# Kernel tuning notes

Measured on AMD Instinct MI355X. Metric: run time of the kernel, lower is better.

## Reference

```python
import jax, jax.numpy as jnp
import numpy as np

WIDTH = 36
N = WIDTH * WIDTH          # 1296 graph nodes per patch
SIGMA = 0.01               # weight_sigma
ZMAX = 0.01                # support_zmax
U_MIN, U_MAX = 0.001, 1.0
N_ITERS = 9                # 1 initial qpsolve + 8 glr refinements


def _build_graph():
    # 4-connected grid graph on WIDTH x WIDTH pixels -> incidence matrix H [E, N]
    nodes = np.arange(N).reshape(WIDTH, WIDTH)
    i0 = np.concatenate([nodes[:, :-1].ravel(), nodes[:-1, :].ravel()])
    i1 = np.concatenate([nodes[:, 1:].ravel(), nodes[1:, :].ravel()])
    E = i0.shape[0]  # 2520
    H = np.zeros((E, N), np.float32)
    H[np.arange(E), i0] = 1.0
    H[np.arange(E), i1] = -1.0
    return i0.astype(np.int32), i1.astype(np.int32), H


def setup_inputs() -> dict:
    key = jax.random.key(0)
    ks = jax.random.split(key, 6)
    B = 2
    i0, i1, H = _build_graph()
    std = 0.02  # weights_init_normal
    return {
        "xf": jax.random.normal(ks[0], (B, 3, WIDTH, WIDTH), jnp.float32),
        "u_param": jax.random.uniform(ks[1], (1,), jnp.float32),
        "H": jnp.asarray(H),
        "cw_in": std * jax.random.normal(ks[2], (32, 3, 3, 3), jnp.float32),
        "b_in": jnp.zeros((32,), jnp.float32),
        "cw_mid": std * jax.random.normal(ks[3], (5, 32, 32, 3, 3), jnp.float32),
        "b_mid": jnp.zeros((5, 32), jnp.float32),
        "cw_out": std * jax.random.normal(ks[4], (6, 32, 3, 3), jnp.float32),
        "b_out": jnp.zeros((6,), jnp.float32),
        "idx0": jnp.asarray(i0),
        "idx1": jnp.asarray(i1),
    }


def _conv(x, w, b):
    y = jax.lax.conv_general_dilated(x, w, (1, 1), "SAME",
                                     dimension_numbers=("NCHW", "OIHW", "NCHW"))
    return y + b[None, :, None, None]


def _cnnf(x, cw_in, b_in, cw_mid, b_mid, cw_out, b_out):
    h = jax.nn.relu(_conv(x, cw_in, b_in))
    for i in range(cw_mid.shape[0]):
        h = jax.nn.relu(_conv(h, cw_mid[i], b_mid[i]))
    return _conv(h, cw_out, b_out)


def _forward(xf, u_param, H, cw_in, b_in, cw_mid, b_mid, cw_out, b_out, idx0, idx1):
    B, C = xf.shape[0], xf.shape[1]
    Ne = idx0.shape[0]
    u = jnp.clip(u_param, U_MIN, U_MAX)[0]  # cnnu == uu(): scalar u, clamped

    y = xf.reshape(B, C, N, 1)
    # edge weights from deep features: w = exp(-sum_f (H f)^2 / sigma^2)
    feat = _cnnf(xf, cw_in, b_in, cw_mid, b_mid, cw_out, b_out).reshape(B, 6, N, 1)
    Fs = jnp.einsum("en,bfno->bfeo", H, feat) ** 2          # [B,6,E,1]
    w = jnp.exp(-Fs.sum(axis=1) / (SIGMA ** 2))              # [B,E,1]
    wv = jnp.broadcast_to(w[:, None, :, 0], (B, C, Ne))      # repeat over channels

    eye = jnp.eye(N, dtype=xf.dtype)
    base = jnp.zeros((B, C, N, N), xf.dtype)                 # base_W

    def step(y):
        z = jnp.einsum("en,bcno->bceo", H, y)                # per-edge diffs [B,C,E,1]
        za = jnp.abs(z[..., 0])                              # [B,C,E]
        Wm = base.at[:, :, idx0, idx1].set(wv).at[:, :, idx1, idx0].set(wv)
        Zm = base.at[:, :, idx0, idx1].set(za).at[:, :, idx1, idx0].set(za)
        Zm = jnp.maximum(Zm, ZMAX)
        Lm = Wm / Zm                                         # reweighted adjacency
        deg = Lm.sum(axis=-1)                                # L @ ones(N,1)
        L = deg[..., :, None] * eye - Lm                     # graph Laplacian
        # qpsolve: GLR closed form  (I + u L) x = y
        return jnp.linalg.solve(eye + u * L, y)

    for _ in range(N_ITERS):
        y = step(y)
    return y.reshape(B, C, WIDTH, WIDTH)


def reference(xf, u_param, H, cw_in, b_in, cw_mid, b_mid, cw_out, b_out, idx0, idx1):
    return _forward(xf, u_param, H, cw_in, b_in, cw_mid, b_mid, cw_out, b_out, idx0, idx1)
```

## Files before the change

kernel.cpp:

```cpp
#include <hip/hip_runtime.h>
#include <math.h>

#define NN 1296
#define OFF 40
#define TOT (OFF + NN + 40)
#define KMAX 240
#define PXW 21

__global__ __launch_bounds__(256) void conv_in_k(
    const float* __restrict__ in, const float* __restrict__ wgt,
    const float* __restrict__ bias, float* __restrict__ out)
{
  const int gid = blockIdx.x * 256 + threadIdx.x;
  const int wid = gid >> 6, lane = gid & 63;
  if (wid >= 2 * 32 * PXW) return;
  const int px = (wid % PXW) * 64 + lane;
  const int co = __builtin_amdgcn_readfirstlane((wid / PXW) % 32);
  const int b  = __builtin_amdgcn_readfirstlane(wid / (PXW * 32));
  if (px >= NN) return;

  const int py = px / 36, pxx = px % 36;
  int offs[9]; float msk[9];
#pragma unroll
  for (int dy = 0; dy < 3; ++dy)
#pragma unroll
    for (int dx = 0; dx < 3; ++dx) {
      const int yy = py + dy - 1, xx = pxx + dx - 1;
      const bool okp = ((unsigned)yy < 36u) && ((unsigned)xx < 36u);
      offs[dy * 3 + dx] = okp ? (yy * 36 + xx) : 0;
      msk[dy * 3 + dx]  = okp ? 1.f : 0.f;
    }

  float acc = bias[co];
  const float* __restrict__ inp = in + (size_t)b * 3 * NN;
  const float* __restrict__ wB  = wgt + (size_t)co * 3 * 9;
#pragma unroll
  for (int ci = 0; ci < 3; ++ci) {
    float v[9];
#pragma unroll
    for (int k9 = 0; k9 < 9; ++k9) v[k9] = msk[k9] * inp[ci * NN + offs[k9]];
#pragma unroll
    for (int k9 = 0; k9 < 9; ++k9) acc = fmaf(v[k9], wB[ci * 9 + k9], acc);
  }
  out[(size_t)(b * 32 + co) * NN + px] = fmaxf(acc, 0.f);
}

__global__ __launch_bounds__(256) void conv_mid2_k(
    const float* __restrict__ in, const float* __restrict__ wgt,
    const float* __restrict__ bias, float* __restrict__ out)
{
  const int blk = blockIdx.x;
  const int pxg = blk % PXW;
  const int cog = (blk / PXW) & 3;
  const int b   = blk / (PXW * 4);
  const int lane = threadIdx.x & 63;
  const int ciq  = __builtin_amdgcn_readfirstlane(threadIdx.x >> 6);
  const int px   = pxg * 64 + lane;
  const bool ok  = px < NN;

  __shared__ float part[4][8][64];

  float acc[8] = {0.f, 0.f, 0.f, 0.f, 0.f, 0.f, 0.f, 0.f};
  if (ok) {
    const int py = px / 36, pxx = px % 36;
    int offs[9]; float msk[9];
#pragma unroll
    for (int dy = 0; dy < 3; ++dy)
#pragma unroll
      for (int dx = 0; dx < 3; ++dx) {
        const int yy = py + dy - 1, xx = pxx + dx - 1;
        const bool okp = ((unsigned)yy < 36u) && ((unsigned)xx < 36u);
        offs[dy * 3 + dx] = okp ? (yy * 36 + xx) : 0;
        msk[dy * 3 + dx]  = okp ? 1.f : 0.f;
      }
    const float* __restrict__ inp = in + ((size_t)b * 32 + ciq * 8) * NN;
    const float* __restrict__ wB = wgt + ((size_t)(cog * 8) * 32 + ciq * 8) * 9;
#pragma unroll
    for (int ci = 0; ci < 8; ++ci) {
      float v[9];
#pragma unroll
      for (int k9 = 0; k9 < 9; ++k9) v[k9] = msk[k9] * inp[ci * NN + offs[k9]];
#pragma unroll
      for (int t = 0; t < 8; ++t)
#pragma unroll
        for (int k9 = 0; k9 < 9; ++k9)
          acc[t] = fmaf(v[k9], wB[(t * 32 + ci) * 9 + k9], acc[t]);
    }
  }
#pragma unroll
  for (int t = 0; t < 8; ++t) part[ciq][t][lane] = acc[t];
  __syncthreads();
  if (ok) {
#pragma unroll
    for (int tt = 0; tt < 2; ++tt) {
      const int t = ciq + tt * 4;
      float s = part[0][t][lane] + part[1][t][lane]
              + part[2][t][lane] + part[3][t][lane] + bias[cog * 8 + t];
      s = fmaxf(s, 0.f);
      out[((size_t)b * 32 + cog * 8 + t) * NN + px] = s;
    }
  }
}

template<int COUT, bool RELU>
__global__ __launch_bounds__(256) void conv_mid_k(
    const float* __restrict__ in, const float* __restrict__ wgt,
    const float* __restrict__ bias, float* __restrict__ out)
{
  const int blk = blockIdx.x;
  const int pxg = blk % PXW;
  const int co  = (blk / PXW) % COUT;
  const int b   = blk / (PXW * COUT);
  const int lane = threadIdx.x & 63;
  const int ciq  = threadIdx.x >> 6;
  const int px   = pxg * 64 + lane;
  const bool ok  = px < NN;

  __shared__ float part[4][64];

  float acc = 0.f;
  if (ok) {
    const int py = px / 36, pxx = px % 36;
    int offs[9]; float msk[9];
#pragma unroll
    for (int dy = 0; dy < 3; ++dy)
#pragma unroll
      for (int dx = 0; dx < 3; ++dx) {
        const int yy = py + dy - 1, xx = pxx + dx - 1;
        const bool okp = ((unsigned)yy < 36u) && ((unsigned)xx < 36u);
        offs[dy * 3 + dx] = okp ? (yy * 36 + xx) : 0;
        msk[dy * 3 + dx]  = okp ? 1.f : 0.f;
      }
    const float* __restrict__ inp = in + ((size_t)b * 32 + ciq * 8) * NN;
    const float* __restrict__ wB  = wgt + ((size_t)co * 32 + ciq * 8) * 9;
#pragma unroll
    for (int ci = 0; ci < 8; ++ci) {
      float v[9];
#pragma unroll
      for (int k9 = 0; k9 < 9; ++k9) v[k9] = msk[k9] * inp[ci * NN + offs[k9]];
#pragma unroll
      for (int k9 = 0; k9 < 9; ++k9) acc = fmaf(v[k9], wB[ci * 9 + k9], acc);
    }
  }
  part[ciq][lane] = acc;
  __syncthreads();
  if (threadIdx.x < 64 && ok) {
    float s = part[0][lane] + part[1][lane] + part[2][lane] + part[3][lane]
            + bias[co];
    if (RELU) s = fmaxf(s, 0.f);
    out[((size_t)b * COUT + co) * NN + px] = s;
  }
}

__global__ __launch_bounds__(384) void gtv_k(
    const float* __restrict__ xf, const float* __restrict__ up,
    const float* __restrict__ feat, float* __restrict__ out)
{
  const int sys = blockIdx.x, b = sys / 3, ch = sys % 3;
  const int tid = threadIdx.x;
  const int wave = tid >> 6, lane = tid & 63;
  const bool act = tid < 324;
  const int qq = act ? tid : 0;
  const int i0 = OFF + 4 * qq;

  __shared__ __align__(16) float ysL[TOT], ahL[TOT], avL[TOT],
                                 dA[TOT], dB[TOT], dgL[TOT];
  __shared__ float red[16];

  float u = up[0]; u = fminf(fmaxf(u, 0.001f), 1.0f);

  if (tid < OFF) {
    const int t2 = OFF + NN + tid;
    ysL[tid] = 0.f; ahL[tid] = 0.f; avL[tid] = 0.f;
    dA[tid] = 0.f; dB[tid] = 0.f; dgL[tid] = 0.f;
    ysL[t2] = 0.f; ahL[t2] = 0.f; avL[t2] = 0.f;
    dA[t2] = 0.f; dB[t2] = 0.f; dgL[t2] = 0.f;
  }

  const float* __restrict__ xfB = xf + (size_t)(b * 3 + ch) * NN;
  float wh4[4] = {0.f, 0.f, 0.f, 0.f}, wv4[4] = {0.f, 0.f, 0.f, 0.f};
  if (act) {
    *(float4*)&ysL[i0] = *(const float4*)&xfB[4 * qq];
#pragma unroll
    for (int j = 0; j < 4; ++j) {
      const int n = 4 * qq + j;
      const int col = n % 36, row = n / 36;
      float sh = 0.f, sv = 0.f;
#pragma unroll
      for (int f = 0; f < 6; ++f) {
        const float* __restrict__ fp = feat + (size_t)(b * 6 + f) * NN;
        const float a = fp[n];
        if (col < 35) { const float d = a - fp[n + 1];  sh += d * d; }
        if (row < 35) { const float d = a - fp[n + 36]; sv += d * d; }
      }
      wh4[j] = (col < 35) ? expf(-sh * 1e4f) : 0.f;
      wv4[j] = (row < 35) ? expf(-sv * 1e4f) : 0.f;
    }
  }
  __syncthreads();

  float x[4] = {0.f, 0.f, 0.f, 0.f};

  for (int it = 0; it < 9; ++it) {
    float4 yv = make_float4(0,0,0,0);
    float ah[4] = {0,0,0,0}, av[4] = {0,0,0,0};
    if (act) {
      yv = *(const float4*)&ysL[i0];
      const float yR = ysL[i0 + 4];
      const float4 yD = *(const float4*)&ysL[i0 + 36];
      ah[0] = u * wh4[0] / fmaxf(fabsf(yv.x - yv.y), 0.01f);
      ah[1] = u * wh4[1] / fmaxf(fabsf(yv.y - yv.z), 0.01f);
      ah[2] = u * wh4[2] / fmaxf(fabsf(yv.z - yv.w), 0.01f);
      ah[3] = u * wh4[3] / fmaxf(fabsf(yv.w - yR  ), 0.01f);
      av[0] = u * wv4[0] / fmaxf(fabsf(yv.x - yD.x), 0.01f);
      av[1] = u * wv4[1] / fmaxf(fabsf(yv.y - yD.y), 0.01f);
      av[2] = u * wv4[2] / fmaxf(fabsf(yv.z - yD.z), 0.01f);
      av[3] = u * wv4[3] / fmaxf(fabsf(yv.w - yD.w), 0.01f);
      *(float4*)&ahL[i0] = make_float4(ah[0], ah[1], ah[2], ah[3]);
      *(float4*)&avL[i0] = make_float4(av[0], av[1], av[2], av[3]);
    }
    __syncthreads();

    float cL[4], cR[4], cU[4], cD[4], cc[4], bn[4], os[4];
    float mo = 0.f;
    if (act) {
      const float cl0 = ahL[i0 - 1];
      const float4 aU = *(const float4*)&avL[i0 - 36];
      cL[0] = cl0;  cL[1] = ah[0]; cL[2] = ah[1]; cL[3] = ah[2];
      cR[0] = ah[0]; cR[1] = ah[1]; cR[2] = ah[2]; cR[3] = ah[3];
      cU[0] = aU.x; cU[1] = aU.y; cU[2] = aU.z; cU[3] = aU.w;
      cD[0] = av[0]; cD[1] = av[1]; cD[2] = av[2]; cD[3] = av[3];
      bn[0] = yv.x; bn[1] = yv.y; bn[2] = yv.z; bn[3] = yv.w;
#pragma unroll
      for (int j = 0; j < 4; ++j) {
        os[j] = cL[j] + cR[j] + cU[j] + cD[j];
        cc[j] = 1.f + os[j];
        mo = fmaxf(mo, os[j]);
      }
      *(float4*)&dA[i0]  = yv;
      *(float4*)&dgL[i0] = make_float4(os[0], os[1], os[2], os[3]);
    } else {
#pragma unroll
      for (int j = 0; j < 4; ++j) {
        cL[j]=cR[j]=cU[j]=cD[j]=0.f; cc[j]=1.f; bn[j]=0.f; os[j]=0.f;
      }
    }
#pragma unroll
    for (int o = 32; o >= 1; o >>= 1) mo = fmaxf(mo, __shfl_xor(mo, o));
    if (lane == 0) red[wave] = mo;
    __syncthreads();

    float me = 0.f;
    if (act) {
      const float dnx3 = dgL[i0 + 4];
      const float4 dwn = *(const float4*)&dgL[i0 + 36];
      const float dn_[4] = { os[1], os[2], os[3], dnx3 };
      const float dd_[4] = { dwn.x, dwn.y, dwn.z, dwn.w };
#pragma unroll
      for (int j = 0; j < 4; ++j)
        me = fmaxf(me, os[j] + fmaxf(dn_[j], dd_[j]));
    }
#pragma unroll
    for (int o = 32; o >= 1; o >>= 1) me = fmaxf(me, __shfl_xor(me, o));
    if (lane == 0) red[8 + wave] = me;
    __syncthreads();
    if (tid == 0) {
      float m1 = red[0], m2 = red[8];
      for (int w = 1; w < 6; ++w) {
        m1 = fmaxf(m1, red[w]); m2 = fmaxf(m2, red[8 + w]);
      }
      red[14] = fminf(2.f * m1, m2);
    }
    __syncthreads();

    const float lmaxL = red[14];
    const float h     = 0.5f * lmaxL;
    const float theta = 1.f + h;
    const float del   = fmaxf(h, 1e-30f);
    const float sig1  = theta / del;
    const float rho0  = del / theta;
    const float kappa = 1.f + lmaxL;
    const float srk   = sqrtf(kappa);
    const float rc    = (srk - 1.f) / (srk + 1.f);

    float r[4], d[4];
    float rmx = 0.f;
    if (act) {
      const float dl = dA[i0 - 1], dr = dA[i0 + 4];
      const float4 u4 = *(const float4*)&dA[i0 - 36];
      const float4 d4 = *(const float4*)&dA[i0 + 36];
      const float uu[4] = {u4.x, u4.y, u4.z, u4.w};
      const float dd[4] = {d4.x, d4.y, d4.z, d4.w};
#pragma unroll
      for (int j = 0; j < 4; ++j) {
        const float nl = (j == 0) ? dl : bn[j - 1];
        const float nr = (j == 3) ? dr : bn[j + 1];
        const float Ab = cc[j] * bn[j] - cL[j] * nl - cR[j] * nr
                       - cU[j] * uu[j] - cD[j] * dd[j];
        x[j] = bn[j];
        r[j] = bn[j] - Ab;
        d[j] = r[j] / theta;
        rmx = fmaxf(rmx, fabsf(r[j]));
      }
      *(float4*)&dB[i0] = make_float4(d[0], d[1], d[2], d[3]);
    } else {
#pragma unroll
      for (int j = 0; j < 4; ++j) { r[j] = 0.f; d[j] = 0.f; x[j] = 0.f; }
    }
#pragma unroll
    for (int o = 32; o >= 1; o >>= 1) rmx = fmaxf(rmx, __shfl_xor(rmx, o));
    if (lane == 0) red[wave] = rmx;
    __syncthreads();
    if (tid == 0) {
      float m = red[0];
      for (int w = 1; w < 6; ++w) m = fmaxf(m, red[w]);
      red[9] = m;
    }
    __syncthreads();

    const float rmax = red[9];
    int kneed;
    if (rmax <= 5e-4f) kneed = 0;
    else if (rc < 1e-10f) kneed = 1;
    else {
      kneed = (int)ceilf(8.0f / (-logf(rc)));
      kneed = (kneed < 1) ? 1 : (kneed > KMAX ? KMAX : kneed);
    }

    float rho = rho0;
    float* dc = dB; float* dnx = dA;
    for (int k = 0; k < kneed; ++k) {
      const float rn = 1.f / (2.f * sig1 - rho);
      const float cd = rn * rho, cr = 2.f * rn / del;
      rho = rn;
      if (act) {
        const float dl = dc[i0 - 1], dr = dc[i0 + 4];
        const float4 u4 = *(const float4*)&dc[i0 - 36];
        const float4 d4 = *(const float4*)&dc[i0 + 36];
        const float uu[4] = {u4.x, u4.y, u4.z, u4.w};
        const float dd[4] = {d4.x, d4.y, d4.z, d4.w};
        float dn[4];
#pragma unroll
        for (int j = 0; j < 4; ++j) {
          const float nl = (j == 0) ? dl : d[j - 1];
          const float nr = (j == 3) ? dr : d[j + 1];
          const float Ad = cc[j] * d[j] - cL[j] * nl - cR[j] * nr
                         - cU[j] * uu[j] - cD[j] * dd[j];
          x[j] += d[j];
          r[j] -= Ad;
          dn[j] = cd * d[j] + cr * r[j];
        }
        *(float4*)&dnx[i0] = make_float4(dn[0], dn[1], dn[2], dn[3]);
#pragma unroll
        for (int j = 0; j < 4; ++j) d[j] = dn[j];
      }
      __syncthreads();
      float* t = dc; dc = dnx; dnx = t;
    }

    if (act) *(float4*)&ysL[i0] = make_float4(x[0], x[1], x[2], x[3]);
    __syncthreads();
  }

  if (act) *(float4*)&out[(size_t)(b * 3 + ch) * NN + 4 * qq]
      = make_float4(x[0], x[1], x[2], x[3]);
}

extern "C" void kernel_launch(void* const* d_in, const int* in_sizes, int n_in,
                              void* d_out, int out_size, void* d_ws, size_t ws_size,
                              hipStream_t stream) {
  const float* xf     = (const float*)d_in[0];
  const float* up     = (const float*)d_in[1];
  const float* cw_in  = (const float*)d_in[3];
  const float* b_in   = (const float*)d_in[4];
  const float* cw_mid = (const float*)d_in[5];
  const float* b_mid  = (const float*)d_in[6];
  const float* cw_out = (const float*)d_in[7];
  const float* b_out  = (const float*)d_in[8];

  float* ws   = (float*)d_ws;
  float* hb0  = ws;
  float* hb1  = hb0 + 82944;
  float* feat = hb1 + 82944;

  conv_in_k<<<dim3(336), dim3(256), 0, stream>>>(xf, cw_in, b_in, hb0);
  const float* src = hb0; float* dst = hb1;
  for (int i = 0; i < 5; ++i) {
    conv_mid2_k<<<dim3(2 * 4 * PXW), dim3(256), 0, stream>>>(
        src, cw_mid + i * 9216, b_mid + i * 32, dst);
    const float* t = dst; dst = (float*)src; src = t;
  }
  conv_mid_k<6, false><<<dim3(2 * 6 * PXW), dim3(256), 0, stream>>>(
      src, cw_out, b_out, feat);

  gtv_k<<<dim3(6), dim3(384), 0, stream>>>(xf, up, feat, (float*)d_out);
}
```

Before: 117.4 us.

## Add residual-based early exit to Chebyshev loop and merge reduction barriers

Stops the Chebyshev iteration early once the max residual, reduced across the block every four steps, falls below a relative tolerance, instead of always running the precomputed iteration cap. Also drops the degree scratch array by recomputing neighbour degrees from edge weights, and replaces single-thread reductions with redundant per-thread reads to remove several barriers. Costs an extra wave reduction every four iterations and makes iteration count data dependent, with looser accuracy control.

```diff
diff --git a/kernel.cpp b/kernel.cpp
--- a/kernel.cpp
+++ b/kernel.cpp
@@ -163,18 +163,15 @@
   const int qq = act ? tid : 0;
   const int i0 = OFF + 4 * qq;
 
-  __shared__ __align__(16) float ysL[TOT], ahL[TOT], avL[TOT],
-                                 dA[TOT], dB[TOT], dgL[TOT];
+  __shared__ __align__(16) float ysL[TOT], ahL[TOT], avL[TOT], dA[TOT], dB[TOT];
   __shared__ float red[16];
 
   float u = up[0]; u = fminf(fmaxf(u, 0.001f), 1.0f);
 
   if (tid < OFF) {
     const int t2 = OFF + NN + tid;
-    ysL[tid] = 0.f; ahL[tid] = 0.f; avL[tid] = 0.f;
-    dA[tid] = 0.f; dB[tid] = 0.f; dgL[tid] = 0.f;
-    ysL[t2] = 0.f; ahL[t2] = 0.f; avL[t2] = 0.f;
-    dA[t2] = 0.f; dB[t2] = 0.f; dgL[t2] = 0.f;
+    ysL[tid] = 0.f; ahL[tid] = 0.f; avL[tid] = 0.f; dA[tid] = 0.f; dB[tid] = 0.f;
+    ysL[t2] = 0.f; ahL[t2] = 0.f; avL[t2] = 0.f; dA[t2] = 0.f; dB[t2] = 0.f;
   }
 
   const float* __restrict__ xfB = xf + (size_t)(b * 3 + ch) * NN;
@@ -202,12 +199,13 @@
   float x[4] = {0.f, 0.f, 0.f, 0.f};
 
   for (int it = 0; it < 9; ++it) {
-    float4 yv = make_float4(0,0,0,0);
+    float4 yv = make_float4(0,0,0,0), yD = make_float4(0,0,0,0);
+    float yR = 0.f;
     float ah[4] = {0,0,0,0}, av[4] = {0,0,0,0};
     if (act) {
       yv = *(const float4*)&ysL[i0];
-      const float yR = ysL[i0 + 4];
-      const float4 yD = *(const float4*)&ysL[i0 + 36];
+      yR = ysL[i0 + 4];
+      yD = *(const float4*)&ysL[i0 + 36];
       ah[0] = u * wh4[0] / fmaxf(fabsf(yv.x - yv.y), 0.01f);
       ah[1] = u * wh4[1] / fmaxf(fabsf(yv.y - yv.z), 0.01f);
       ah[2] = u * wh4[2] / fmaxf(fabsf(yv.z - yv.w), 0.01f);
@@ -222,7 +220,7 @@
     __syncthreads();
 
     float cL[4], cR[4], cU[4], cD[4], cc[4], bn[4], os[4];
-    float mo = 0.f;
+    float mo = 0.f, me = 0.f;
     if (act) {
       const float cl0 = ahL[i0 - 1];
       const float4 aU = *(const float4*)&avL[i0 - 36];
@@ -237,8 +235,22 @@
         cc[j] = 1.f + os[j];
         mo = fmaxf(mo, os[j]);
       }
-      *(float4*)&dA[i0]  = yv;
-      *(float4*)&dgL[i0] = make_float4(os[0], os[1], os[2], os[3]);
+      const float ahR  = ahL[i0 + 4];
+      const float avRu = avL[i0 - 32];
+      const float avR  = avL[i0 + 4];
+      const float osR  = ah[3] + ahR + avRu + avR;
+      const float ahDl = ahL[i0 + 35];
+      const float4 ahD = *(const float4*)&ahL[i0 + 36];
+      const float4 avD = *(const float4*)&avL[i0 + 36];
+      float osD[4];
+      osD[0] = ahDl  + ahD.x + av[0] + avD.x;
+      osD[1] = ahD.x + ahD.y + av[1] + avD.y;
+      osD[2] = ahD.y + ahD.z + av[2] + avD.z;
+      osD[3] = ahD.z + ahD.w + av[3] + avD.w;
+      const float osN[4] = { os[1], os[2], os[3], osR };
+#pragma unroll
+      for (int j = 0; j < 4; ++j)
+        me = fmaxf(me, os[j] + fmaxf(osN[j], osD[j]));
     } else {
 #pragma unroll
       for (int j = 0; j < 4; ++j) {
@@ -246,34 +258,18 @@
       }
     }
 #pragma unroll
-    for (int o = 32; o >= 1; o >>= 1) mo = fmaxf(mo, __shfl_xor(mo, o));
-    if (lane == 0) red[wave] = mo;
+    for (int o = 32; o >= 1; o >>= 1) {
+      mo = fmaxf(mo, __shfl_xor(mo, o));
+      me = fmaxf(me, __shfl_xor(me, o));
+    }
+    if (lane == 0) { red[wave] = mo; red[8 + wave] = me; }
     __syncthreads();
-
-    float me = 0.f;
-    if (act) {
-      const float dnx3 = dgL[i0 + 4];
-      const float4 dwn = *(const float4*)&dgL[i0 + 36];
-      const float dn_[4] = { os[1], os[2], os[3], dnx3 };
-      const float dd_[4] = { dwn.x, dwn.y, dwn.z, dwn.w };
-#pragma unroll
-      for (int j = 0; j < 4; ++j)
-        me = fmaxf(me, os[j] + fmaxf(dn_[j], dd_[j]));
-    }
-#pragma unroll
-    for (int o = 32; o >= 1; o >>= 1) me = fmaxf(me, __shfl_xor(me, o));
-    if (lane == 0) red[8 + wave] = me;
-    __syncthreads();
-    if (tid == 0) {
-      float m1 = red[0], m2 = red[8];
-      for (int w = 1; w < 6; ++w) {
-        m1 = fmaxf(m1, red[w]); m2 = fmaxf(m2, red[8 + w]);
-      }
-      red[14] = fminf(2.f * m1, m2);
-    }
-    __syncthreads();
-
-    const float lmaxL = red[14];
+    float m1 = fmaxf(fmaxf(red[0], red[1]),
+               fmaxf(fmaxf(red[2], red[3]), fmaxf(red[4], red[5])));
+    float m2 = fmaxf(fmaxf(red[8], red[9]),
+               fmaxf(fmaxf(red[10], red[11]), fmaxf(red[12], red[13])));
+    const float lmaxL = fminf(2.f * m1, m2);
+
     const float h     = 0.5f * lmaxL;
     const float theta = 1.f + h;
     const float del   = fmaxf(h, 1e-30f);
@@ -286,15 +282,14 @@
     float r[4], d[4];
     float rmx = 0.f;
     if (act) {
-      const float dl = dA[i0 - 1], dr = dA[i0 + 4];
-      const float4 u4 = *(const float4*)&dA[i0 - 36];
-      const float4 d4 = *(const float4*)&dA[i0 + 36];
-      const float uu[4] = {u4.x, u4.y, u4.z, u4.w};
-      const float dd[4] = {d4.x, d4.y, d4.z, d4.w};
+      const float bl = ysL[i0 - 1];
+      const float4 bu = *(const float4*)&ysL[i0 - 36];
+      const float uu[4] = {bu.x, bu.y, bu.z, bu.w};
+      const float dd[4] = {yD.x, yD.y, yD.z, yD.w};
 #pragma unroll
       for (int j = 0; j < 4; ++j) {
-        const float nl = (j == 0) ? dl : bn[j - 1];
-        const float nr = (j == 3) ? dr : bn[j + 1];
+        const float nl = (j == 0) ? bl : bn[j - 1];
+        const float nr = (j == 3) ? yR : bn[j + 1];
         const float Ab = cc[j] * bn[j] - cL[j] * nl - cR[j] * nr
                        - cU[j] * uu[j] - cD[j] * dd[j];
         x[j] = bn[j];
@@ -311,25 +306,26 @@
     for (int o = 32; o >= 1; o >>= 1) rmx = fmaxf(rmx, __shfl_xor(rmx, o));
     if (lane == 0) red[wave] = rmx;
     __syncthreads();
-    if (tid == 0) {
-      float m = red[0];
-      for (int w = 1; w < 6; ++w) m = fmaxf(m, red[w]);
-      red[9] = m;
-    }
-    __syncthreads();
-
-    const float rmax = red[9];
-    int kneed;
-    if (rmax <= 5e-4f) kneed = 0;
-    else if (rc < 1e-10f) kneed = 1;
+    const float rmax0 = fmaxf(fmaxf(red[0], red[1]),
+                       fmaxf(fmaxf(red[2], red[3]), fmaxf(red[4], red[5])));
+
+    int kcap;
+    if (rmax0 <= 5e-4f) kcap = 0;
+    else if (rc < 1e-10f) kcap = 1;
     else {
-      kneed = (int)ceilf(8.0f / (-logf(rc)));
-      kneed = (kneed < 1) ? 1 : (kneed > KMAX ? KMAX : kneed);
-    }
+      kcap = (int)ceilf(8.0f / (-logf(rc)));
+      kcap = (kcap < 1) ? 1 : (kcap > KMAX ? KMAX : kcap);
+    }
+    const float eps = fmaxf(rmax0 * 3.3e-4f, 2.5e-4f);
 
     float rho = rho0;
     float* dc = dB; float* dnx = dA;
-    for (int k = 0; k < kneed; ++k) {
+    for (int k = 0; k < kcap; ++k) {
+      if (k >= 4 && (k & 3) == 0) {
+        const float rmc = fmaxf(fmaxf(red[0], red[1]),
+                         fmaxf(fmaxf(red[2], red[3]), fmaxf(red[4], red[5])));
+        if (rmc <= eps) break;
+      }
       const float rn = 1.f / (2.f * sig1 - rho);
       const float cd = rn * rho, cr = 2.f * rn / del;
       rho = rn;
@@ -353,6 +349,16 @@
         *(float4*)&dnx[i0] = make_float4(dn[0], dn[1], dn[2], dn[3]);
 #pragma unroll
         for (int j = 0; j < 4; ++j) d[j] = dn[j];
+      }
+      if ((k & 3) == 3) {
+        float rm = 0.f;
+        if (act) {
+          rm = fmaxf(fmaxf(fabsf(r[0]), fabsf(r[1])),
+                     fmaxf(fabsf(r[2]), fabsf(r[3])));
+        }
+#pragma unroll
+        for (int o = 32; o >= 1; o >>= 1) rm = fmaxf(rm, __shfl_xor(rm, o));
+        if (lane == 0) red[wave] = rm;
       }
       __syncthreads();
       float* t = dc; dc = dnx; dnx = t;
```

Result: slower. 121.9 us (+3.8%).
